# Kernel tuning notes

Measured on AMD Instinct MI355X. Metric: run time of the kernel, lower is better.

The kernel has to match this reference:

```python
import jax, jax.numpy as jnp
import numpy as np

B, S, H, T = 32, 512, 1024, 32


def setup_inputs() -> dict:
    key = jax.random.key(0)
    ks = jax.random.split(key, 8)
    hidden = jax.random.normal(ks[0], (B, S, H), dtype=jnp.float32)
    W = jax.random.normal(ks[1], (H, T), dtype=jnp.float32) * 0.02
    b = jax.random.normal(ks[2], (T,), dtype=jnp.float32) * 0.02
    start_trans = jax.random.normal(ks[3], (T,), dtype=jnp.float32) * 0.1
    end_trans = jax.random.normal(ks[4], (T,), dtype=jnp.float32) * 0.1
    trans = jax.random.normal(ks[5], (T, T), dtype=jnp.float32) * 0.1
    tags = jax.random.randint(ks[6], (B, S), 0, T, dtype=jnp.int64)
    # variable-length mask: first position always valid (CRF requirement)
    lengths = jax.random.randint(ks[7], (B,), S // 2, S + 1)
    mask = jnp.arange(S)[None, :] < lengths[:, None]  # [B,S] bool
    return {"hidden": hidden, "W": W, "b": b, "start_trans": start_trans,
            "end_trans": end_trans, "trans": trans, "tags": tags, "mask": mask}


def reference(hidden, W, b, start_trans, end_trans, trans, tags, mask):
    # emission = log_softmax(fc(last_hidden_state))  [B,S,T]
    emissions = jax.nn.log_softmax(jnp.einsum('bsh,ht->bst', hidden, W) + b, axis=-1)
    maskf = mask.astype(emissions.dtype)

    # --- numerator: score of the gold tag path ---
    emit_tag = jnp.take_along_axis(emissions, tags[..., None], axis=-1)[..., 0]  # [B,S]
    trans_tag = trans[tags[:, :-1], tags[:, 1:]]                                  # [B,S-1]
    num = (start_trans[tags[:, 0]]
           + (emit_tag * maskf).sum(axis=1)
           + (trans_tag * maskf[:, 1:]).sum(axis=1))
    seq_len = mask.sum(axis=1).astype(jnp.int32)                                  # [B]
    last_tags = jnp.take_along_axis(tags, (seq_len - 1)[:, None].astype(tags.dtype), axis=1)[:, 0]
    num = num + end_trans[last_tags]

    # --- denominator: forward algorithm (masked logsumexp recurrence) ---
    alpha0 = start_trans[None, :] + emissions[:, 0]  # [B,T]

    def step(alpha, inp):
        em_t, m_t = inp  # [B,T], [B]
        nxt = jax.nn.logsumexp(alpha[:, :, None] + trans[None] + em_t[:, None, :], axis=1)
        return jnp.where(m_t[:, None], nxt, alpha), None

    em_rest = jnp.moveaxis(emissions[:, 1:], 1, 0)  # [S-1,B,T]
    m_rest = jnp.moveaxis(mask[:, 1:], 1, 0)        # [S-1,B]
    alpha, _ = jax.lax.scan(step, alpha0, (em_rest, m_rest))
    denom = jax.nn.logsumexp(alpha + end_trans[None], axis=1)  # [B]

    llh = num - denom        # CRF returns per-batch log-likelihood
    return -llh.mean()       # loss = (-crf(...)).mean()
```

## Files before the change

### kernel.cpp

```cpp
#include <hip/hip_runtime.h>
#include <hip/hip_bf16.h>


#define Bb 32
#define Ss 512
#define Hh 1024
#define Tt 32
#define NROWS (Bb*Ss)
#define NCHUNK 32
#define CHUNK_L 16
#define NSUP 8

typedef __attribute__((ext_vector_type(8))) short bf16x8;
typedef __attribute__((ext_vector_type(4))) float f32x4;

__device__ __forceinline__ short f2bf(float f) {
  union { float f; unsigned u; } v; v.f = f;
  unsigned u = v.u;
  return (short)((u + 0x7FFFu + ((u >> 16) & 1u)) >> 16);
}
__device__ __forceinline__ float bf2f(short s) {
  union { unsigned u; float f; } v;
  v.u = ((unsigned)(unsigned short)s) << 16;
  return v.f;
}

__global__ __launch_bounds__(128) void wpack_kernel(
    const float* __restrict__ W, short* __restrict__ Wpk,
    float* __restrict__ out) {
  const int k = blockIdx.x * 128 + threadIdx.x;
  if (k == 0) out[0] = 0.f;
#pragma unroll
  for (int t = 0; t < 32; ++t)
    Wpk[t * Hh + k] = f2bf(W[k * 32 + t]);
}

__global__ __launch_bounds__(256) void emis_fused_kernel(
    const float* __restrict__ hidden, const short* __restrict__ Wpk,
    const float* __restrict__ bias, float* __restrict__ logem) {
  __shared__ __align__(16) char smem[32768];
  float* red = (float*)smem;
  const int tid = threadIdx.x;
  const int wv = tid >> 6, lane = tid & 63;
  const int n = lane & 15, q = lane >> 4;
  const int row0 = blockIdx.x * 16;
  const int koff = wv * 256;

  {
    const int skc = (tid >> 3) & 7;
    const int sq = (tid >> 1) & 3;
    const int sj0 = (tid & 1) * 4;
    const int rbase = (tid >> 6) * 8192 + skc * 1024 + sj0 * 2;
    const int uxor = skc * 32;
    const float* hp = hidden + (size_t)row0 * Hh + 4 * tid;
#pragma unroll
    for (int i = 0; i < 16; ++i) {
      const float4 v = *(const float4*)(hp + (size_t)i * Hh);
      uint2 u;
      u.x = (unsigned short)f2bf(v.x) | ((unsigned)(unsigned short)f2bf(v.y) << 16);
      u.y = (unsigned short)f2bf(v.z) | ((unsigned)(unsigned short)f2bf(v.w) << 16);
      const int unit = ((i * 4 + sq) * 16) ^ uxor;
      *(uint2*)(smem + rbase + unit) = u;
    }
  }
  __syncthreads();

  const short* bpl = Wpk + n * Hh + koff;
  const short* bpr = Wpk + (16 + n) * Hh + koff;
  f32x4 d0 = {0.f, 0.f, 0.f, 0.f}, d1 = {0.f, 0.f, 0.f, 0.f};
#pragma unroll
  for (int kc = 0; kc < 8; ++kc) {
    const int aaddr = wv * 8192 + kc * 1024 + (((n * 4 + q) * 16) ^ (kc * 32));
    const bf16x8 a = *(const bf16x8*)(smem + aaddr);
    const bf16x8 wl = *(const bf16x8*)(bpl + kc * 32 + 8 * q);
    const bf16x8 wr = *(const bf16x8*)(bpr + kc * 32 + 8 * q);
    d0 = __builtin_amdgcn_mfma_f32_16x16x32_bf16(a, wl, d0, 0, 0, 0);
    d1 = __builtin_amdgcn_mfma_f32_16x16x32_bf16(a, wr, d1, 0, 0, 0);
  }
  __syncthreads();

#pragma unroll
  for (int r = 0; r < 4; ++r) {
    red[(wv * 16 + 4 * q + r) * 33 + n] = d0[r];
    red[(wv * 16 + 4 * q + r) * 33 + 16 + n] = d1[r];
  }
  __syncthreads();

  const int row = tid >> 4, c0 = tid & 15, c1 = 16 + c0;
  float v0 = 0.f, v1 = 0.f;
#pragma unroll
  for (int w = 0; w < 4; ++w) {
    v0 += red[(w * 16 + row) * 33 + c0];
    v1 += red[(w * 16 + row) * 33 + c1];
  }
  const float L0 = v0 + bias[c0], L1 = v1 + bias[c1];
  float mx = fmaxf(L0, L1);
#pragma unroll
  for (int d = 8; d >= 1; d >>= 1) mx = fmaxf(mx, __shfl_xor(mx, d, 16));
  float se = __expf(L0 - mx) + __expf(L1 - mx);
#pragma unroll
  for (int d = 8; d >= 1; d >>= 1) se += __shfl_xor(se, d, 16);
  const float corr = mx + __logf(se);
  const size_t rb = (size_t)(row0 + row) * Tt;
  logem[rb + c0] = L0 - corr;
  logem[rb + c1] = L1 - corr;
}

__device__ __forceinline__ void combine32(
    const short* __restrict__ Ea, const short* __restrict__ Eb,
    const float* __restrict__ Oa, const float* __restrict__ Ob, float obmax,
    int n, int q,
    f32x4& c00, f32x4& c01, f32x4& c10, f32x4& c11,
    float* __restrict__ lgn0, float* __restrict__ lgn1,
    float* __restrict__ iv0, float* __restrict__ iv1) {
  const bf16x8 a0 = *(const bf16x8*)(Ea + n * 40 + 8 * q);
  const bf16x8 a1 = *(const bf16x8*)(Ea + (16 + n) * 40 + 8 * q);
  bf16x8 bL, bR;
#pragma unroll
  for (int jj = 0; jj < 8; ++jj) {
    const float sc = __expf(Ob[8 * q + jj] - obmax);
    bL[jj] = f2bf(bf2f(Eb[(8 * q + jj) * 40 + n]) * sc);
    bR[jj] = f2bf(bf2f(Eb[(8 * q + jj) * 40 + 16 + n]) * sc);
  }
  const f32x4 z = {0.f, 0.f, 0.f, 0.f};
  c00 = __builtin_amdgcn_mfma_f32_16x16x32_bf16(a0, bL, z, 0, 0, 0);
  c01 = __builtin_amdgcn_mfma_f32_16x16x32_bf16(a0, bR, z, 0, 0, 0);
  c10 = __builtin_amdgcn_mfma_f32_16x16x32_bf16(a1, bL, z, 0, 0, 0);
  c11 = __builtin_amdgcn_mfma_f32_16x16x32_bf16(a1, bR, z, 0, 0, 0);
#pragma unroll
  for (int r = 0; r < 4; ++r) {
    float m0v = fmaxf(c00[r], c01[r]);
    float m1v = fmaxf(c10[r], c11[r]);
#pragma unroll
    for (int d = 8; d >= 1; d >>= 1) {
      m0v = fmaxf(m0v, __shfl_xor(m0v, d, 16));
      m1v = fmaxf(m1v, __shfl_xor(m1v, d, 16));
    }
    m0v = fmaxf(m0v, 1e-37f);
    m1v = fmaxf(m1v, 1e-37f);
    iv0[r] = __builtin_amdgcn_rcpf(m0v);
    iv1[r] = __builtin_amdgcn_rcpf(m1v);
    lgn0[r] = Oa[4 * q + r] + obmax + __logf(m0v);
    lgn1[r] = Oa[16 + 4 * q + r] + obmax + __logf(m1v);
  }
}

__global__ __launch_bounds__(256) void chunk_kernel(
    const float* __restrict__ logem, const float* __restrict__ trans,
    const int* __restrict__ mask, float* __restrict__ ecT4,
    float* __restrict__ moff4, float* __restrict__ cmax4) {
  __shared__ __align__(16) float Pbuf[4][32 * 36];
  __shared__ __align__(16) short Ebuf[4][32][40];
  __shared__ float Obuf[4][32];
  __shared__ float Cmx[4];
  const int tid = threadIdx.x;
  const int wv = tid >> 6, lane = tid & 63;
  const int n = lane & 15, q = lane >> 4;
  const int chunk = blockIdx.x * 4 + wv;
  const int b = chunk >> 5, cc = chunk & 31;
  float* P = &Pbuf[wv][0];

  float etr0[8], etr1[8];
#pragma unroll
  for (int jj = 0; jj < 8; ++jj) {
    etr0[jj] = __expf(trans[(8 * q + jj) * 32 + n]);
    etr1[jj] = __expf(trans[(8 * q + jj) * 32 + 16 + n]);
  }

  const int t0 = 1 + cc * CHUNK_L;
  const int rowbase = b * Ss + t0;
  int pred = 0;
  if (lane < 16 && t0 + lane < Ss) pred = mask[rowbase + lane];
  const unsigned long long bal = __ballot(pred != 0);
  const int nst = __popcll(bal & 0xFFFFull);

  bf16x8 a0, a1;
#pragma unroll
  for (int jj = 0; jj < 8; ++jj) {
    a0[jj] = (n == 8 * q + jj) ? (short)0x3F80 : (short)0;
    a1[jj] = (16 + n == 8 * q + jj) ? (short)0x3F80 : (short)0;
  }

  f32x4 d00, d01, d10, d11;
  if (nst == 0) {
#pragma unroll
    for (int r = 0; r < 4; ++r) {
      d00[r] = (4 * q + r == n) ? 1.f : 0.f;
      d01[r] = 0.f;
      d10[r] = 0.f;
      d11[r] = (4 * q + r == n) ? 1.f : 0.f;
    }
  }
  float em0 = 0.f, em1 = 0.f;
  if (nst > 0) {
    em0 = __expf(logem[(size_t)rowbase * Tt + n]);
    em1 = __expf(logem[(size_t)rowbase * Tt + 16 + n]);
  }
  for (int st = 0; st < nst; ++st) {
    float em0n = 0.f, em1n = 0.f;
    if (st + 1 < nst) {
      em0n = __expf(logem[(size_t)(rowbase + st + 1) * Tt + n]);
      em1n = __expf(logem[(size_t)(rowbase + st + 1) * Tt + 16 + n]);
    }
    bf16x8 bL, bR;
#pragma unroll
    for (int jj = 0; jj < 8; ++jj) {
      bL[jj] = f2bf(etr0[jj] * em0);
      bR[jj] = f2bf(etr1[jj] * em1);
    }
    const f32x4 z = {0.f, 0.f, 0.f, 0.f};
    d00 = __builtin_amdgcn_mfma_f32_16x16x32_bf16(a0, bL, z, 0, 0, 0);
    d01 = __builtin_amdgcn_mfma_f32_16x16x32_bf16(a0, bR, z, 0, 0, 0);
    d10 = __builtin_amdgcn_mfma_f32_16x16x32_bf16(a1, bL, z, 0, 0, 0);
    d11 = __builtin_amdgcn_mfma_f32_16x16x32_bf16(a1, bR, z, 0, 0, 0);
    if (st + 1 < nst) {
#pragma unroll
      for (int r = 0; r < 4; ++r) {
        P[(4 * q + r) * 36 + n] = d00[r];
        P[(4 * q + r) * 36 + 16 + n] = d01[r];
        P[(16 + 4 * q + r) * 36 + n] = d10[r];
        P[(16 + 4 * q + r) * 36 + 16 + n] = d11[r];
      }
      asm volatile("s_waitcnt lgkmcnt(0)" ::: "memory");
      __builtin_amdgcn_sched_barrier(0);
      const float4 lo0 = *(const float4*)&P[n * 36 + 8 * q];
      const float4 lo1 = *(const float4*)&P[n * 36 + 8 * q + 4];
      const float4 hi0 = *(const float4*)&P[(16 + n) * 36 + 8 * q];
      const float4 hi1 = *(const float4*)&P[(16 + n) * 36 + 8 * q + 4];
      a0[0] = f2bf(lo0.x); a0[1] = f2bf(lo0.y); a0[2] = f2bf(lo0.z); a0[3] = f2bf(lo0.w);
      a0[4] = f2bf(lo1.x); a0[5] = f2bf(lo1.y); a0[6] = f2bf(lo1.z); a0[7] = f2bf(lo1.w);
      a1[0] = f2bf(hi0.x); a1[1] = f2bf(hi0.y); a1[2] = f2bf(hi0.z); a1[3] = f2bf(hi0.w);
      a1[4] = f2bf(hi1.x); a1[5] = f2bf(hi1.y); a1[6] = f2bf(hi1.z); a1[7] = f2bf(hi1.w);
    }
    em0 = em0n; em1 = em1n;
  }

  {
    float lg0[4], lg1[4], iv0[4], iv1[4];
#pragma unroll
    for (int r = 0; r < 4; ++r) {
      float m0v = fmaxf(d00[r], d01[r]);
      float m1v = fmaxf(d10[r], d11[r]);
#pragma unroll
      for (int d = 8; d >= 1; d >>= 1) {
        m0v = fmaxf(m0v, __shfl_xor(m0v, d, 16));
        m1v = fmaxf(m1v, __shfl_xor(m1v, d, 16));
      }
      m0v = fmaxf(m0v, 1e-37f);
      m1v = fmaxf(m1v, 1e-37f);
      lg0[r] = __logf(m0v); iv0[r] = __builtin_amdgcn_rcpf(m0v);
      lg1[r] = __logf(m1v); iv1[r] = __builtin_amdgcn_rcpf(m1v);
    }
#pragma unroll
    for (int r = 0; r < 4; ++r) {
      Ebuf[wv][4 * q + r][n] = f2bf(d00[r] * iv0[r]);
      Ebuf[wv][4 * q + r][16 + n] = f2bf(d01[r] * iv0[r]);
      Ebuf[wv][16 + 4 * q + r][n] = f2bf(d10[r] * iv1[r]);
      Ebuf[wv][16 + 4 * q + r][16 + n] = f2bf(d11[r] * iv1[r]);
    }
    if (n == 0) {
#pragma unroll
      for (int r = 0; r < 4; ++r) {
        Obuf[wv][4 * q + r] = lg0[r];
        Obuf[wv][16 + 4 * q + r] = lg1[r];
      }
    }
    float cm = fmaxf(fmaxf(fmaxf(lg0[0], lg0[1]), fmaxf(lg0[2], lg0[3])),
                     fmaxf(fmaxf(lg1[0], lg1[1]), fmaxf(lg1[2], lg1[3])));
    cm = fmaxf(cm, __shfl_xor(cm, 16));
    cm = fmaxf(cm, __shfl_xor(cm, 32));
    if (lane == 0) Cmx[wv] = cm;
  }
  __syncthreads();

  if (wv < 2) {
    const int ai = 2 * wv, bi = 2 * wv + 1;
    f32x4 c00, c01, c10, c11;
    float lg0[4], lg1[4], iv0[4], iv1[4];
    combine32(&Ebuf[ai][0][0], &Ebuf[bi][0][0], Obuf[ai], Obuf[bi], Cmx[bi],
              n, q, c00, c01, c10, c11, lg0, lg1, iv0, iv1);
#pragma unroll
    for (int r = 0; r < 4; ++r) {
      Ebuf[ai][4 * q + r][n] = f2bf(c00[r] * iv0[r]);
      Ebuf[ai][4 * q + r][16 + n] = f2bf(c01[r] * iv0[r]);
      Ebuf[ai][16 + 4 * q + r][n] = f2bf(c10[r] * iv1[r]);
      Ebuf[ai][16 + 4 * q + r][16 + n] = f2bf(c11[r] * iv1[r]);
    }
    if (n == 0) {
#pragma unroll
      for (int r = 0; r < 4; ++r) {
        Obuf[ai][4 * q + r] = lg0[r];
        Obuf[ai][16 + 4 * q + r] = lg1[r];
      }
    }
    float cm = fmaxf(fmaxf(fmaxf(lg0[0], lg0[1]), fmaxf(lg0[2], lg0[3])),
                     fmaxf(fmaxf(lg1[0], lg1[1]), fmaxf(lg1[2], lg1[3])));
    cm = fmaxf(cm, __shfl_xor(cm, 16));
    cm = fmaxf(cm, __shfl_xor(cm, 32));
    if (lane == 0) Cmx[ai] = cm;
  }
  __syncthreads();

  if (wv == 0) {
    f32x4 c00, c01, c10, c11;
    float lg0[4], lg1[4], iv0[4], iv1[4];
    combine32(&Ebuf[0][0][0], &Ebuf[2][0][0], Obuf[0], Obuf[2], Cmx[2],
              n, q, c00, c01, c10, c11, lg0, lg1, iv0, iv1);
    const int sup = blockIdx.x;
    float* E = ecT4 + (size_t)sup * 32 * 32;
    {
      float4 s;
      s = make_float4(c00[0] * iv0[0], c00[1] * iv0[1], c00[2] * iv0[2], c00[3] * iv0[3]);
      *(float4*)&E[n * 32 + 4 * q] = s;
      s = make_float4(c10[0] * iv1[0], c10[1] * iv1[1], c10[2] * iv1[2], c10[3] * iv1[3]);
      *(float4*)&E[n * 32 + 16 + 4 * q] = s;
      s = make_float4(c01[0] * iv0[0], c01[1] * iv0[1], c01[2] * iv0[2], c01[3] * iv0[3]);
      *(float4*)&E[(16 + n) * 32 + 4 * q] = s;
      s = make_float4(c11[0] * iv1[0], c11[1] * iv1[1], c11[2] * iv1[2], c11[3] * iv1[3]);
      *(float4*)&E[(16 + n) * 32 + 16 + 4 * q] = s;
    }
    if (n == 0) {
      float* Mo = moff4 + (size_t)sup * 32;
      *(float4*)&Mo[4 * q] = make_float4(lg0[0], lg0[1], lg0[2], lg0[3]);
      *(float4*)&Mo[16 + 4 * q] = make_float4(lg1[0], lg1[1], lg1[2], lg1[3]);
    }
    float cm = fmaxf(fmaxf(fmaxf(lg0[0], lg0[1]), fmaxf(lg0[2], lg0[3])),
                     fmaxf(fmaxf(lg1[0], lg1[1]), fmaxf(lg1[2], lg1[3])));
    cm = fmaxf(cm, __shfl_xor(cm, 16));
    cm = fmaxf(cm, __shfl_xor(cm, 32));
    if (lane == 0) cmax4[sup] = cm;
  }
}

__global__ __launch_bounds__(64) void phase2_kernel(
    const float* __restrict__ logem, const float* __restrict__ start_trans,
    const float* __restrict__ end_trans, const float* __restrict__ ecT4,
    const float* __restrict__ moff4, const float* __restrict__ cmax4,
    const float* __restrict__ trans, const int* __restrict__ tags,
    const int* __restrict__ mask, float* __restrict__ out) {
  const int b = blockIdx.x;
  const int lane = threadIdx.x;
  const int j = lane & 31;
  __shared__ __align__(16) float qlds[32];

  const int base_row = b * Ss;
  int lensum = 0;
  float snum = 0.f;
#pragma unroll
  for (int k = 0; k < 8; ++k) {
    const int ss = lane + 64 * k;
    const int m = mask[base_row + ss];
    lensum += m;
    if (m) {
      const int tg = tags[base_row + ss];
      snum += logem[(size_t)(base_row + ss) * Tt + tg];
      if (ss > 0) snum += trans[tags[base_row + ss - 1] * Tt + tg];
    }
  }
#pragma unroll
  for (int d = 32; d >= 1; d >>= 1) {
    snum += __shfl_xor(snum, d);
    lensum += __shfl_xor(lensum, d);
  }

  const float* base = ecT4 + (size_t)b * NSUP * 32 * 32;
  const float* mbase = moff4 + (size_t)b * NSUP * 32;
  const float cm_l = (j < NSUP) ? cmax4[b * NSUP + j] : 0.f;

  float4 M[8], N[8];
  const float* r0 = base + j * 32;
#pragma unroll
  for (int k = 0; k < 8; ++k) M[k] = *(const float4*)(r0 + 4 * k);
  float mo_cur = mbase[j];

  float al0 = start_trans[j] + logem[(size_t)base_row * Tt + j];
  float m0 = al0;
#pragma unroll
  for (int d = 16; d >= 1; d >>= 1) m0 = fmaxf(m0, __shfl_xor(m0, d, 32));
  float a = __expf(al0 - m0);
  float Mb = m0;
  const float eend = __expf(end_trans[j]);

  float mo_next = 0.f;
  for (int c = 0; c < NSUP; ++c) {
    if (c + 1 < NSUP) {
      const float* rn = base + ((c + 1) * 32 + j) * 32;
#pragma unroll
      for (int k = 0; k < 8; ++k) N[k] = *(const float4*)(rn + 4 * k);
      mo_next = mbase[(c + 1) * 32 + j];
    }
    const float mom = __shfl(cm_l, c, 32);
    const float qv = a * __expf(mo_cur - mom);
    if (lane < 32) qlds[j] = qv;
    asm volatile("s_waitcnt lgkmcnt(0)" ::: "memory");
    __builtin_amdgcn_sched_barrier(0);
    float s0 = 0.f, s1 = 0.f, s2 = 0.f, s3 = 0.f;
#pragma unroll
    for (int k = 0; k < 8; ++k) {
      const float4 q4 = *(const float4*)(qlds + 4 * k);
      float* sp = (k & 1) ? ((k & 2) ? &s3 : &s1) : ((k & 2) ? &s2 : &s0);
      *sp = fmaf(q4.x, M[k].x, *sp);
      *sp = fmaf(q4.y, M[k].y, *sp);
      *sp = fmaf(q4.z, M[k].z, *sp);
      *sp = fmaf(q4.w, M[k].w, *sp);
    }
    const float s = (s0 + s1) + (s2 + s3);
    Mb += mom;
    if ((c & 3) == 3) {
      float m = s;
#pragma unroll
      for (int d = 16; d >= 1; d >>= 1) m = fmaxf(m, __shfl_xor(m, d, 32));
      m = fmaxf(m, 1e-30f);
      a = s * __builtin_amdgcn_rcpf(m);
      Mb += __logf(m);
    } else {
      a = s;
    }
#pragma unroll
    for (int k = 0; k < 8; ++k) M[k] = N[k];
    mo_cur = mo_next;
  }
  float z = a * eend;
#pragma unroll
  for (int d = 16; d >= 1; d >>= 1) z += __shfl_xor(z, d, 32);
  if (lane == 0) {
    const float numfull = snum + start_trans[tags[base_row]] +
                          end_trans[tags[base_row + lensum - 1]];
    const float denom = Mb + __logf(z);
    atomicAdd(out, -(numfull - denom) * (1.0f / 32.0f));
  }
}

extern "C" void kernel_launch(void* const* d_in, const int* in_sizes, int n_in,
                              void* d_out, int out_size, void* d_ws, size_t ws_size,
                              hipStream_t stream) {
  const float* hidden = (const float*)d_in[0];
  const float* W = (const float*)d_in[1];
  const float* bias = (const float*)d_in[2];
  const float* start_trans = (const float*)d_in[3];
  const float* end_trans = (const float*)d_in[4];
  const float* trans = (const float*)d_in[5];
  const int* tags = (const int*)d_in[6];
  const int* mask = (const int*)d_in[7];
  float* out = (float*)d_out;

  float* logem = (float*)d_ws;
  float* ecT4 = logem + (size_t)NROWS * Tt;
  float* moff4 = ecT4 + (size_t)Bb * NSUP * 32 * 32;
  float* cmax4 = moff4 + (size_t)Bb * NSUP * 32;
  short* Wpk = (short*)(cmax4 + (size_t)Bb * NSUP);

  wpack_kernel<<<8, 128, 0, stream>>>(W, Wpk, out);
  emis_fused_kernel<<<NROWS / 16, 256, 0, stream>>>(hidden, Wpk, bias, logem);
  chunk_kernel<<<Bb * NCHUNK / 4, 256, 0, stream>>>(logem, trans, mask,
                                                    ecT4, moff4, cmax4);
  phase2_kernel<<<Bb, 64, 0, stream>>>(logem, start_trans, end_trans, ecT4,
                                       moff4, cmax4, trans, tags, mask, out);
}
```

Baseline: 140.8 us.

## Split each chunk into two interleaved 8-step halves for ILP

Each wave now runs two independent transfer-matrix product chains (first and second halves of its 16-step chunk) interleaved in one loop, then combines them with an extra combine32 pass. The intermediate product is stored to shared memory directly as bf16 and reloaded as a bf16x8 vector, removing the fp32 staging buffer and the per-element conversions on reload. The aim is to halve the serial MFMA/LDS dependency chain length and hide latency, at the cost of more registers and an extra combine step with a block barrier.

```diff
diff --git a/kernel.cpp b/kernel.cpp
--- a/kernel.cpp
+++ b/kernel.cpp
@@ -145,20 +145,69 @@
   }
 }
 
+__device__ __forceinline__ void half_epilogue(
+    f32x4 d00, f32x4 d01, f32x4 d10, f32x4 d11, int nst,
+    int n, int q, int lane, short* __restrict__ E,
+    float* __restrict__ O, float* __restrict__ cmxp) {
+  if (nst == 0) {
+#pragma unroll
+    for (int r = 0; r < 4; ++r) {
+      d00[r] = (4 * q + r == n) ? 1.f : 0.f;
+      d01[r] = 0.f;
+      d10[r] = 0.f;
+      d11[r] = (4 * q + r == n) ? 1.f : 0.f;
+    }
+  }
+  float lg0[4], lg1[4], iv0[4], iv1[4];
+#pragma unroll
+  for (int r = 0; r < 4; ++r) {
+    float m0v = fmaxf(d00[r], d01[r]);
+    float m1v = fmaxf(d10[r], d11[r]);
+#pragma unroll
+    for (int d = 8; d >= 1; d >>= 1) {
+      m0v = fmaxf(m0v, __shfl_xor(m0v, d, 16));
+      m1v = fmaxf(m1v, __shfl_xor(m1v, d, 16));
+    }
+    m0v = fmaxf(m0v, 1e-37f);
+    m1v = fmaxf(m1v, 1e-37f);
+    lg0[r] = __logf(m0v); iv0[r] = __builtin_amdgcn_rcpf(m0v);
+    lg1[r] = __logf(m1v); iv1[r] = __builtin_amdgcn_rcpf(m1v);
+  }
+#pragma unroll
+  for (int r = 0; r < 4; ++r) {
+    E[(4 * q + r) * 40 + n] = f2bf(d00[r] * iv0[r]);
+    E[(4 * q + r) * 40 + 16 + n] = f2bf(d01[r] * iv0[r]);
+    E[(16 + 4 * q + r) * 40 + n] = f2bf(d10[r] * iv1[r]);
+    E[(16 + 4 * q + r) * 40 + 16 + n] = f2bf(d11[r] * iv1[r]);
+  }
+  if (n == 0) {
+#pragma unroll
+    for (int r = 0; r < 4; ++r) {
+      O[4 * q + r] = lg0[r];
+      O[16 + 4 * q + r] = lg1[r];
+    }
+  }
+  float cm = fmaxf(fmaxf(fmaxf(lg0[0], lg0[1]), fmaxf(lg0[2], lg0[3])),
+                   fmaxf(fmaxf(lg1[0], lg1[1]), fmaxf(lg1[2], lg1[3])));
+  cm = fmaxf(cm, __shfl_xor(cm, 16));
+  cm = fmaxf(cm, __shfl_xor(cm, 32));
+  if (lane == 0) *cmxp = cm;
+}
+
 __global__ __launch_bounds__(256) void chunk_kernel(
     const float* __restrict__ logem, const float* __restrict__ trans,
     const int* __restrict__ mask, float* __restrict__ ecT4,
     float* __restrict__ moff4, float* __restrict__ cmax4) {
-  __shared__ __align__(16) float Pbuf[4][32 * 36];
-  __shared__ __align__(16) short Ebuf[4][32][40];
-  __shared__ float Obuf[4][32];
-  __shared__ float Cmx[4];
+  __shared__ __align__(16) short Ebuf[4][2][32][40];
+  __shared__ float Obuf[4][2][32];
+  __shared__ float Cmx[4][2];
   const int tid = threadIdx.x;
   const int wv = tid >> 6, lane = tid & 63;
   const int n = lane & 15, q = lane >> 4;
   const int chunk = blockIdx.x * 4 + wv;
   const int b = chunk >> 5, cc = chunk & 31;
-  float* P = &Pbuf[wv][0];
+  short* PA = &Ebuf[wv][0][0][0];
+  short* PB = &Ebuf[wv][1][0][0];
 
   float etr0[8], etr1[8];
 #pragma unroll
@@ -169,107 +218,137 @@
 
   const int t0 = 1 + cc * CHUNK_L;
   const int rowbase = b * Ss + t0;
+  const int rowbaseB = rowbase + 8;
   int pred = 0;
   if (lane < 16 && t0 + lane < Ss) pred = mask[rowbase + lane];
   const unsigned long long bal = __ballot(pred != 0);
   const int nst = __popcll(bal & 0xFFFFull);
-
-  bf16x8 a0, a1;
+  const int nstA = nst < 8 ? nst : 8;
+  const int nstB = nst > 8 ? nst - 8 : 0;
+
+  bf16x8 aA0, aA1, aB0, aB1;
 #pragma unroll
   for (int jj = 0; jj < 8; ++jj) {
-    a0[jj] = (n == 8 * q + jj) ? (short)0x3F80 : (short)0;
-    a1[jj] = (16 + n == 8 * q + jj) ? (short)0x3F80 : (short)0;
-  }
-
-  f32x4 d00, d01, d10, d11;
-  if (nst == 0) {
-#pragma unroll
-    for (int r = 0; r < 4; ++r) {
-      d00[r] = (4 * q + r == n) ? 1.f : 0.f;
-      d01[r] = 0.f;
-      d10[r] = 0.f;
-      d11[r] = (4 * q + r == n) ? 1.f : 0.f;
-    }
-  }
-  float em0 = 0.f, em1 = 0.f;
-  if (nst > 0) {
-    em0 = __expf(logem[(size_t)rowbase * Tt + n]);
-    em1 = __expf(logem[(size_t)rowbase * Tt + 16 + n]);
-  }
-  for (int st = 0; st < nst; ++st) {
-    float em0n = 0.f, em1n = 0.f;
-    if (st + 1 < nst) {
-      em0n = __expf(logem[(size_t)(rowbase + st + 1) * Tt + n]);
-      em1n = __expf(logem[(size_t)(rowbase + st + 1) * Tt + 16 + n]);
-    }
-    bf16x8 bL, bR;
-#pragma unroll
-    for (int jj = 0; jj < 8; ++jj) {
-      bL[jj] = f2bf(etr0[jj] * em0);
-      bR[jj] = f2bf(etr1[jj] * em1);
+    const short ilo = (n == 8 * q + jj) ? (short)0x3F80 : (short)0;
+    const short ihi = (16 + n == 8 * q + jj) ? (short)0x3F80 : (short)0;
+    aA0[jj] = ilo; aA1[jj] = ihi;
+    aB0[jj] = ilo; aB1[jj] = ihi;
+  }
+
+  f32x4 dA00 = {0,0,0,0}, dA01 = {0,0,0,0}, dA10 = {0,0,0,0}, dA11 = {0,0,0,0};
+  f32x4 dB00 = {0,0,0,0}, dB01 = {0,0,0,0}, dB10 = {0,0,0,0}, dB11 = {0,0,0,0};
+
+  float emA0 = 0.f, emA1 = 0.f, emB0 = 0.f, emB1 = 0.f;
+  if (nstA > 0) {
+    emA0 = __expf(logem[(size_t)rowbase * Tt + n]);
+    emA1 = __expf(logem[(size_t)rowbase * Tt + 16 + n]);
+  }
+  if (nstB > 0) {
+    emB0 = __expf(logem[(size_t)rowbaseB * Tt + n]);
+    emB1 = __expf(logem[(size_t)rowbaseB * Tt + 16 + n]);
+  }
+
+  const int nmax = nstA > nstB ? nstA : nstB;
+  for (int st = 0; st < nmax; ++st) {
+    float emA0n = 0.f, emA1n = 0.f, emB0n = 0.f, emB1n = 0.f;
+    if (st + 1 < nstA) {
+      emA0n = __expf(logem[(size_t)(rowbase + st + 1) * Tt + n]);
+      emA1n = __expf(logem[(size_t)(rowbase + st + 1) * Tt + 16 + n]);
+    }
+    if (st + 1 < nstB) {
+      emB0n = __expf(logem[(size_t)(rowbaseB + st + 1) * Tt + n]);
+      emB1n = __expf(logem[(size_t)(rowbaseB + st + 1) * Tt + 16 + n]);
     }
     const f32x4 z = {0.f, 0.f, 0.f, 0.f};
-    d00 = __builtin_amdgcn_mfma_f32_16x16x32_bf16(a0, bL, z, 0, 0, 0);
-    d01 = __builtin_amdgcn_mfma_f32_16x16x32_bf16(a0, bR, z, 0, 0, 0);
-    d10 = __builtin_amdgcn_mfma_f32_16x16x32_bf16(a1, bL, z, 0, 0, 0);
-    d11 = __builtin_amdgcn_mfma_f32_16x16x32_bf16(a1, bR, z, 0, 0, 0);
-    if (st + 1 < nst) {
+    if (st < nstA) {
+      bf16x8 bL, bR;
+#pragma unroll
+      for (int jj = 0; jj < 8; ++jj) {
+        bL[jj] = f2bf(etr0[jj] * emA0);
+        bR[jj] = f2bf(etr1[jj] * emA1);
+      }
+      dA00 = __builtin_amdgcn_mfma_f32_16x16x32_bf16(aA0, bL, z, 0, 0, 0);
+      dA01 = __builtin_amdgcn_mfma_f32_16x16x32_bf16(aA0, bR, z, 0, 0, 0);
+      dA10 = __builtin_amdgcn_mfma_f32_16x16x32_bf16(aA1, bL, z, 0, 0, 0);
+      dA11 = __builtin_amdgcn_mfma_f32_16x16x32_bf16(aA1, bR, z, 0, 0, 0);
+    }
+    if (st < nstB) {
+      bf16x8 bL, bR;
+#pragma unroll
+      for (int jj = 0; jj < 8; ++jj) {
+        bL[jj] = f2bf(etr0[jj] * emB0);
+        bR[jj] = f2bf(etr1[jj] * emB1);
+      }
+      dB00 = __builtin_amdgcn_mfma_f32_16x16x32_bf16(aB0, bL, z, 0, 0, 0);
+      dB01 = __builtin_amdgcn_mfma_f32_16x16x32_bf16(aB0, bR, z, 0, 0, 0);
+      dB10 = __builtin_amdgcn_mfma_f32_16x16x32_bf16(aB1, bL, z, 0, 0, 0);
+      dB11 = __builtin_amdgcn_mfma_f32_16x16x32_bf16(aB1, bR, z, 0, 0, 0);
+    }
+    const bool wA = (st + 1 < nstA), wB = (st + 1 < nstB);
+    if (wA) {
 #pragma unroll
       for (int r = 0; r < 4; ++r) {
-        P[(4 * q + r) * 36 + n] = d00[r];
-        P[(4 * q + r) * 36 + 16 + n] = d01[r];
-        P[(16 + 4 * q + r) * 36 + n] = d10[r];
-        P[(16 + 4 * q + r) * 36 + 16 + n] = d11[r];
+        PA[(4 * q + r) * 40 + n] = f2bf(dA00[r]);
+        PA[(4 * q + r) * 40 + 16 + n] = f2bf(dA01[r]);
+        PA[(16 + 4 * q + r) * 40 + n] = f2bf(dA10[r]);
+        PA[(16 + 4 * q + r) * 40 + 16 + n] = f2bf(dA11[r]);
       }
+    }
+    if (wB) {
+#pragma unroll
+      for (int r = 0; r < 4; ++r) {
+        PB[(4 * q + r) * 40 + n] = f2bf(dB00[r]);
+        PB[(4 * q + r) * 40 + 16 + n] = f2bf(dB01[r]);
+        PB[(16 + 4 * q + r) * 40 + n] = f2bf(dB10[r]);
+        PB[(16 + 4 * q + r) * 40 + 16 + n] = f2bf(dB11[r]);
+      }
+    }
+    if (wA | wB) {
       asm volatile("s_waitcnt lgkmcnt(0)" ::: "memory");
       __builtin_amdgcn_sched_barrier(0);
-      const float4 lo0 = *(const float4*)&P[n * 36 + 8 * q];
-      const float4 lo1 = *(const float4*)&P[n * 36 + 8 * q + 4];
-      const float4 hi0 = *(const float4*)&P[(16 + n) * 36 + 8 * q];
-      const float4 hi1 = *(const float4*)&P[(16 + n) * 36 + 8 * q + 4];
-      a0[0] = f2bf(lo0.x); a0[1] = f2bf(lo0.y); a0[2] = f2bf(lo0.z); a0[3] = f2bf(lo0.w);
-      a0[4] = f2bf(lo1.x); a0[5] = f2bf(lo1.y); a0[6] = f2bf(lo1.z); a0[7] = f2bf(lo1.w);
-      a1[0] = f2bf(hi0.x); a1[1] = f2bf(hi0.y); a1[2] = f2bf(hi0.z); a1[3] = f2bf(hi0.w);
-      a1[4] = f2bf(hi1.x); a1[5] = f2bf(hi1.y); a1[6] = f2bf(hi1.z); a1[7] = f2bf(hi1.w);
-    }
-    em0 = em0n; em1 = em1n;
-  }
+    }
+    if (wA) {
+      aA0 = *(const bf16x8*)(PA + n * 40 + 8 * q);
+      aA1 = *(const bf16x8*)(PA + (16 + n) * 40 + 8 * q);
+    }
+    if (wB) {
+      aB0 = *(const bf16x8*)(PB + n * 40 + 8 * q);
+      aB1 = *(const bf16x8*)(PB + (16 + n) * 40 + 8 * q);
+    }
+    emA0 = emA0n; emA1 = emA1n; emB0 = emB0n; emB1 = emB1n;
+  }
+
+  half_epilogue(dA00, dA01, dA10, dA11, nstA, n, q, lane,
+                &Ebuf[wv][0][0][0], Obuf[wv][0], &Cmx[wv][0]);
+  half_epilogue(dB00, dB01, dB10, dB11, nstB, n, q, lane,
+                &Ebuf[wv][1][0][0], Obuf[wv][1], &Cmx[wv][1]);
+  __syncthreads();
 
   {
+    f32x4 c00, c01, c10, c11;
     float lg0[4], lg1[4], iv0[4], iv1[4];
+    combine32(&Ebuf[wv][0][0][0], &Ebuf[wv][1][0][0],
+              Obuf[wv][0], Obuf[wv][1], Cmx[wv][1],
+              n, q, c00, c01, c10, c11, lg0, lg1, iv0, iv1);
 #pragma unroll
     for (int r = 0; r < 4; ++r) {
-      float m0v = fmaxf(d00[r], d01[r]);
-      float m1v = fmaxf(d10[r], d11[r]);
-#pragma unroll
-      for (int d = 8; d >= 1; d >>= 1) {
-        m0v = fmaxf(m0v, __shfl_xor(m0v, d, 16));
-        m1v = fmaxf(m1v, __shfl_xor(m1v, d, 16));
-      }
-      m0v = fmaxf(m0v, 1e-37f);
-      m1v = fmaxf(m1v, 1e-37f);
-      lg0[r] = __logf(m0v); iv0[r] = __builtin_amdgcn_rcpf(m0v);
-      lg1[r] = __logf(m1v); iv1[r] = __builtin_amdgcn_rcpf(m1v);
-    }
-#pragma unroll
-    for (int r = 0; r < 4; ++r) {
-      Ebuf[wv][4 * q + r][n] = f2bf(d00[r] * iv0[r]);
-      Ebuf[wv][4 * q + r][16 + n] = f2bf(d01[r] * iv0[r]);
-      Ebuf[wv][16 + 4 * q + r][n] = f2bf(d10[r] * iv1[r]);
-      Ebuf[wv][16 + 4 * q + r][16 + n] = f2bf(d11[r] * iv1[r]);
+      Ebuf[wv][0][4 * q + r][n] = f2bf(c00[r] * iv0[r]);
+      Ebuf[wv][0][4 * q + r][16 + n] = f2bf(c01[r] * iv0[r]);
+      Ebuf[wv][0][16 + 4 * q + r][n] = f2bf(c10[r] * iv1[r]);
+      Ebuf[wv][0][16 + 4 * q + r][16 + n] = f2bf(c11[r] * iv1[r]);
     }
     if (n == 0) {
 #pragma unroll
       for (int r = 0; r < 4; ++r) {
-        Obuf[wv][4 * q + r] = lg0[r];
-        Obuf[wv][16 + 4 * q + r] = lg1[r];
+        Obuf[wv][0][4 * q + r] = lg0[r];
+        Obuf[wv][0][16 + 4 * q + r] = lg1[r];
       }
     }
     float cm = fmaxf(fmaxf(fmaxf(lg0[0], lg0[1]), fmaxf(lg0[2], lg0[3])),
                      fmaxf(fmaxf(lg1[0], lg1[1]), fmaxf(lg1[2], lg1[3])));
     cm = fmaxf(cm, __shfl_xor(cm, 16));
     cm = fmaxf(cm, __shfl_xor(cm, 32));
-    if (lane == 0) Cmx[wv] = cm;
+    if (lane == 0) Cmx[wv][0] = cm;
   }
   __syncthreads();
 
@@ -277,34 +356,36 @@
     const int ai = 2 * wv, bi = 2 * wv + 1;
     f32x4 c00, c01, c10, c11;
     float lg0[4], lg1[4], iv0[4], iv1[4];
-    combine32(&Ebuf[ai][0][0], &Ebuf[bi][0][0], Obuf[ai], Obuf[bi], Cmx[bi],
+    combine32(&Ebuf[ai][0][0][0], &Ebuf[bi][0][0][0],
+              Obuf[ai][0], Obuf[bi][0], Cmx[bi][0],
               n, q, c00, c01, c10, c11, lg0, lg1, iv0, iv1);
 #pragma unroll
     for (int r = 0; r < 4; ++r) {
-      Ebuf[ai][4 * q + r][n] = f2bf(c00[r] * iv0[r]);
-      Ebuf[ai][4 * q + r][16 + n] = f2bf(c01[r] * iv0[r]);
-      Ebuf[ai][16 + 4 * q + r][n] = f2bf(c10[r] * iv1[r]);
-      Ebuf[ai][16 + 4 * q + r][16 + n] = f2bf(c11[r] * iv1[r]);
+      Ebuf[ai][0][4 * q + r][n] = f2bf(c00[r] * iv0[r]);
+      Ebuf[ai][0][4 * q + r][16 + n] = f2bf(c01[r] * iv0[r]);
+      Ebuf[ai][0][16 + 4 * q + r][n] = f2bf(c10[r] * iv1[r]);
+      Ebuf[ai][0][16 + 4 * q + r][16 + n] = f2bf(c11[r] * iv1[r]);
     }
     if (n == 0) {
 #pragma unroll
       for (int r = 0; r < 4; ++r) {
-        Obuf[ai][4 * q + r] = lg0[r];
-        Obuf[ai][16 + 4 * q + r] = lg1[r];
+        Obuf[ai][0][4 * q + r] = lg0[r];
+        Obuf[ai][0][16 + 4 * q + r] = lg1[r];
       }
     }
     float cm = fmaxf(fmaxf(fmaxf(lg0[0], lg0[1]), fmaxf(lg0[2], lg0[3])),
                      fmaxf(fmaxf(lg1[0], lg1[1]), fmaxf(lg1[2], lg1[3])));
     cm = fmaxf(cm, __shfl_xor(cm, 16));
     cm = fmaxf(cm, __shfl_xor(cm, 32));
-    if (lane == 0) Cmx[ai] = cm;
+    if (lane == 0) Cmx[ai][0] = cm;
   }
   __syncthreads();
 
   if (wv == 0) {
     f32x4 c00, c01, c10, c11;
     float lg0[4], lg1[4], iv0[4], iv1[4];
-    combine32(&Ebuf[0][0][0], &Ebuf[2][0][0], Obuf[0], Obuf[2], Cmx[2],
+    combine32(&Ebuf[0][0][0][0], &Ebuf[2][0][0][0],
+              Obuf[0][0], Obuf[2][0], Cmx[2][0],
               n, q, c00, c01, c10, c11, lg0, lg1, iv0, iv1);
     const int sup = blockIdx.x;
     float* E = ecT4 + (size_t)sup * 32 * 32;
```

Result: slower. 144.8 us (+2.9%).
